# Optimization experiments

Measured on AMD Instinct MI355X. Metric: run time of the kernel, lower is better.

The kernel has to match this reference:

```python
import jax, jax.numpy as jnp
import numpy as np

B, O, H, I = 256, 128, 1024, 2048  # batch, objects, hidden, input_size
Hh = H // 2  # 512; x_j feature dim
DF = I - Hh  # 1536; X_F feature dim


def _xavier(key, shape):
    fan_in, fan_out = shape[1], shape[0]
    lim = np.sqrt(6.0 / (fan_in + fan_out))
    return jax.random.uniform(key, shape, jnp.float32, -lim, lim)


def setup_inputs() -> dict:
    key = jax.random.key(0)
    ks = jax.random.split(key, 24)
    mask = jax.random.bernoulli(ks[0], 0.7, (B, O))
    mask = mask.at[:, 0].set(True)  # ensure at least one valid object per row
    inp = {
        "x_j": jax.random.normal(ks[1], (B, O, Hh), jnp.float32),
        "x_mask": mask,
        "X_F": jax.random.normal(ks[2], (B, DF), jnp.float32),
        "h": jax.random.normal(ks[3], (B, 1, H), jnp.float32),
        "c": jax.random.normal(ks[4], (B, 1, H), jnp.float32),
    }
    names_W = ["W_i", "W_f", "W_c", "W_o"]
    names_U = ["U_i", "U_f", "U_c", "U_o"]
    names_V = ["V_i", "V_f", "V_c", "V_o"]
    k = 5
    for n in names_W:
        inp[n] = _xavier(ks[k], (H, I)); k += 1
    for n in names_U + names_V:
        inp[n] = _xavier(ks[k], (H, H)); k += 1
    for n in ["b_i", "b_f", "b_c", "b_o"]:
        inp[n] = jnp.zeros((H,), jnp.float32)
    inp["w"] = _xavier(ks[k], (1, Hh)); k += 1
    inp["W_e"] = _xavier(ks[k], (Hh, H)); k += 1
    inp["U_e"] = _xavier(ks[k], (Hh, Hh)); k += 1
    inp["b_e"] = jnp.zeros((Hh,), jnp.float32)
    return inp


def reference(x_j, x_mask, X_F, h, c,
              W_i, W_f, W_c, W_o,
              U_i, U_f, U_c, U_o,
              V_i, V_f, V_c, V_o,
              b_i, b_f, b_c, b_o,
              w, W_e, U_e, b_e):
    # Additive attention over objects.
    # h: (B,1,H) -> (B,1,Hh) broadcasts against x_j proj (B,O,Hh)
    e = jnp.tanh(h @ W_e.T + x_j @ U_e.T + b_e)      # (B,O,Hh)
    e = (e @ w.T)[..., 0]                              # (B,O)
    e = jnp.where(x_mask, e, -1e9)
    a = jax.nn.softmax(e, axis=1)                      # (B,O)
    phi_j = jnp.einsum('bo,bok->bk', a, x_j)[:, None, :]  # (B,1,Hh)
    x = jnp.concatenate([phi_j, X_F[:, None, :]], axis=2)  # (B,1,I)

    # Peephole LSTM gates (h, c: (B,1,H))
    i = jax.nn.sigmoid(x @ W_i.T + h @ U_i.T + c @ V_i.T + b_i)
    f = jax.nn.sigmoid(x @ W_f.T + h @ U_f.T + c @ V_f.T + b_f)
    new_c = f * c + i * jnp.tanh(x @ W_c.T + h @ U_c.T + b_c)
    o = jax.nn.sigmoid(x @ W_o.T + h @ U_o.T + c @ V_o.T + b_o)
    new_h = o * jnp.tanh(new_c)
    return new_h, new_c
```

## Files before the change

kernel.cpp:

```cpp
#include <hip/hip_runtime.h>
#include <hip/hip_bf16.h>

typedef unsigned char u8;
typedef unsigned short u16;
typedef unsigned int u32;
typedef __attribute__((ext_vector_type(8))) short bf8;
typedef __attribute__((ext_vector_type(4))) float f4;

#define B_ 256
#define O_ 128
#define Hh_ 512
#define H_ 1024
#define DF_ 1536
#define I_ 2048

#define HWE_OFF   0
#define XC_OFF    524288
#define PRE_OFF   2621440
#define FLAG_OFF  6815744

__device__ __forceinline__ float bflo(u32 u){ union{u32 i; float f;} v; v.i = u<<16; return v.f; }
__device__ __forceinline__ float bfhi(u32 u){ union{u32 i; float f;} v; v.i = u & 0xffff0000u; return v.f; }
__device__ __forceinline__ float bf1(u16 u){ union{u32 i; float f;} v; v.i = ((u32)u)<<16; return v.f; }
__device__ __forceinline__ u16 f2bf(float f){
    __hip_bfloat16 h = __float2bfloat16(f);
    union{ __hip_bfloat16 h; u16 u; } v; v.h = h; return v.u;
}
__device__ __forceinline__ u32 pack2(float a, float b){
    return ((u32)f2bf(a)) | (((u32)f2bf(b))<<16);
}
__device__ __forceinline__ uint4 load8(const void* p, size_t idx, int isf32){
    if(isf32){
        const float4* f = (const float4*)((const float*)p + idx);
        float4 x = f[0], y = f[1];
        uint4 r;
        r.x = pack2(x.x, x.y); r.y = pack2(x.z, x.w);
        r.z = pack2(y.x, y.y); r.w = pack2(y.z, y.w);
        return r;
    }
    return *(const uint4*)((const u16*)p + idx);
}
__device__ __forceinline__ float loads(const void* p, size_t idx, int isf32){
    return isf32 ? ((const float*)p)[idx] : bf1(((const u16*)p)[idx]);
}
__device__ __forceinline__ float fast_tanh(float x){
    return 1.0f - 2.0f/(__expf(2.0f*x)+1.0f);
}
__device__ __forceinline__ float sigmoidf_(float x){
    return 1.0f/(1.0f+__expf(-x));
}

__global__ void k_detect(const u8* __restrict__ m, const u16* __restrict__ xj,
                         int* __restrict__ flags){
    __shared__ int n1, n2, n3, mb, xo;
    int t = threadIdx.x;
    if(t==0){ n1=0; n2=0; n3=0; mb=0; xo=0; }
    __syncthreads();
    int a1=0, a2=0, a3=0, amax=0;
    for(int i=t; i<8192; i+=256){
        int v = m[i]; int c = i&3;
        if(c==1) a1|=v;
        if(c==2) a2|=v;
        if(c==3) a3|=v;
        amax = amax > v ? amax : v;
    }
    if(a1) atomicOr(&n1,1);
    if(a2) atomicOr(&n2,1);
    if(a3) atomicOr(&n3,1);
    atomicMax(&mb, amax);
    int e = 0;
    for(int i=t; i<2048; i+=256){
        u32 u = xj[2*i];
        int ex = (u>>7)&0xFF;
        if(ex >= 156) e = 1;
    }
    if(e) atomicOr(&xo,1);
    __syncthreads();
    if(t==0){
        int w;
        if(!n1 && !n2 && !n3)      w = 4;
        else if(!n1 && n2 && n3)   w = 4;
        else if(mb > 1)            w = 2;
        else                       w = 1;
        flags[0] = w;
        flags[1] = xo;
    }
}

__global__ __launch_bounds__(256) void k_hwe(const void* __restrict__ h,
                                             const void* __restrict__ We,
                                             const int* __restrict__ flags,
                                             float* __restrict__ hwe){
    int n0 = blockIdx.x*64;
    int kc = blockIdx.y*256;
    int m0 = blockIdx.z*128;
    int t = threadIdx.x;
    int isf32 = flags[1];
    __shared__ __align__(16) u16 As[128*40];
    __shared__ __align__(16) u16 Bs[64*40];
    int w = t>>6, lane = t&63;
    int q = lane>>4, l16 = lane&15;
    int koff = q*8;
    f4 acc[2][4];
    for(int mi=0;mi<2;mi++) for(int ni=0;ni<4;ni++){
        f4 z = {0.f,0.f,0.f,0.f}; acc[mi][ni] = z;
    }
    for(int ks=0; ks<256; ks+=32){
        __syncthreads();
        for(int i=0;i<2;i++){
            int row = i*64 + (t>>2), cv = t&3;
            uint4 va = load8(h, (size_t)(m0+row)*H_ + kc + ks + cv*8, isf32);
            *(uint4*)&As[row*40 + cv*8] = va;
        }
        {
            int row = t>>2, cv = t&3;
            uint4 vb = load8(We, (size_t)(n0+row)*H_ + kc + ks + cv*8, isf32);
            *(uint4*)&Bs[row*40 + cv*8] = vb;
        }
        __syncthreads();
        bf8 af[2], bfr[4];
        for(int mi=0;mi<2;mi++) af[mi]  = *(const bf8*)&As[(w*32+mi*16+l16)*40 + koff];
        for(int ni=0;ni<4;ni++) bfr[ni] = *(const bf8*)&Bs[(ni*16+l16)*40 + koff];
        for(int mi=0;mi<2;mi++)
            for(int ni=0;ni<4;ni++)
                acc[mi][ni] = __builtin_amdgcn_mfma_f32_16x16x32_bf16(af[mi], bfr[ni], acc[mi][ni], 0,0,0);
    }
    for(int mi=0;mi<2;mi++){
        for(int r=0;r<4;r++){
            int brow = m0 + w*32 + mi*16 + q*4 + r;
            for(int ni=0;ni<4;ni++){
                int ncol = n0 + ni*16 + l16;
                atomicAdd(&hwe[(size_t)brow*Hh_ + ncol], acc[mi][ni][r]);
            }
        }
    }
}

__global__ __launch_bounds__(256) void k_pack(const void* __restrict__ XF,
                                              const void* __restrict__ h,
                                              const void* __restrict__ c,
                                              const int* __restrict__ flags,
                                              u16* __restrict__ Xc){
    int b = blockIdx.y;
    int r = blockIdx.x*256 + threadIdx.x;
    int isf32 = flags[1];
    float v;
    if(r < DF_)            v = loads(XF, (size_t)b*DF_ + r, isf32);
    else if(r < DF_ + H_)  v = loads(h,  (size_t)b*H_ + (r - DF_), isf32);
    else                   v = loads(c,  (size_t)b*H_ + (r - DF_ - H_), isf32);
    Xc[(size_t)b*4096 + 512 + r] = f2bf(v);
}

__global__ __launch_bounds__(256) void k_attn(const void* __restrict__ xj,
                                              const void* __restrict__ wvec,
                                              const void* __restrict__ Ue,
                                              const void* __restrict__ be,
                                              const float* __restrict__ hwe,
                                              const int* __restrict__ flags,
                                              float* __restrict__ Epart){
    int b = blockIdx.x, nc = blockIdx.y, t = threadIdx.x;
    int isf32 = flags[1];
    __shared__ __align__(16) u16 As[128*40];
    __shared__ __align__(16) u16 Bs[128*40];
    __shared__ float hwes[128];
    __shared__ float wvs[128];
    __shared__ float es[O_];

    if(t < 128){
        int col = nc*128 + t;
        hwes[t] = hwe[(size_t)b*Hh_ + col] + loads(be, col, isf32);
        wvs[t]  = loads(wvec, col, isf32);
    }
    if(t < O_) es[t] = 0.f;

    const size_t xboff = (size_t)b*O_*Hh_;

    int w = t>>6, lane = t&63;
    int wm = w>>1, wn = w&1;
    int q = lane>>4, l16 = lane&15;
    int koff = q*8;

    f4 acc[4][4];
    for(int mi=0;mi<4;mi++) for(int ni=0;ni<4;ni++){
        f4 z = {0.f,0.f,0.f,0.f}; acc[mi][ni] = z;
    }
    for(int ks=0; ks<Hh_; ks+=32){
        __syncthreads();
        for(int i=0;i<2;i++){
            int qq = t + i*256;
            int row = qq>>2, cv = qq&3;
            uint4 va = load8(xj, xboff + (size_t)row*Hh_ + ks + cv*8, isf32);
            *(uint4*)&As[row*40 + cv*8] = va;
            uint4 vb = load8(Ue, (size_t)(nc*128 + row)*Hh_ + ks + cv*8, isf32);
            *(uint4*)&Bs[row*40 + cv*8] = vb;
        }
        __syncthreads();
        bf8 af[4], bfr[4];
        for(int mi=0;mi<4;mi++) af[mi]  = *(const bf8*)&As[(wm*64+mi*16+l16)*40 + koff];
        for(int ni=0;ni<4;ni++) bfr[ni] = *(const bf8*)&Bs[(wn*64+ni*16+l16)*40 + koff];
        for(int mi=0;mi<4;mi++)
            for(int ni=0;ni<4;ni++)
                acc[mi][ni] = __builtin_amdgcn_mfma_f32_16x16x32_bf16(af[mi], bfr[ni], acc[mi][ni], 0,0,0);
    }
    for(int mi=0;mi<4;mi++){
        for(int r=0;r<4;r++){
            int o = wm*64 + mi*16 + q*4 + r;
            float part = 0.f;
            for(int ni=0;ni<4;ni++){
                int col = wn*64 + ni*16 + l16;
                part += wvs[col] * fast_tanh(hwes[col] + acc[mi][ni][r]);
            }
            part += __shfl_xor(part, 1);
            part += __shfl_xor(part, 2);
            part += __shfl_xor(part, 4);
            part += __shfl_xor(part, 8);
            if(l16 == 0) atomicAdd(&es[o], part);
        }
    }
    __syncthreads();
    if(t < O_) Epart[(size_t)nc*32768 + (size_t)b*O_ + t] = es[t];
}

__global__ __launch_bounds__(512) void k_soft(const float* __restrict__ Epart,
                                              const void* __restrict__ maskp,
                                              const void* __restrict__ xj,
                                              const int* __restrict__ flags,
                                              u16* __restrict__ Xc){
    int b = blockIdx.x, t = threadIdx.x;
    int isf32 = flags[1];
    int mw = flags[0];
    __shared__ float es[O_];
    __shared__ float as_[O_];
    __shared__ float red[2];
    if(t < O_){
        float e = Epart[(size_t)b*O_ + t]
                + Epart[32768 + (size_t)b*O_ + t]
                + Epart[2*32768 + (size_t)b*O_ + t]
                + Epart[3*32768 + (size_t)b*O_ + t];
        size_t mi_ = (size_t)b*O_ + t;
        bool valid;
        if(mw == 1)      valid = ((const u8*)maskp)[mi_]  != 0;
        else if(mw == 2) valid = ((const u16*)maskp)[mi_] != 0;
        else             valid = ((const u32*)maskp)[mi_] != 0;
        es[t] = valid ? e : -1e30f;
    }
    __syncthreads();
    if(t < 64){
        float v = fmaxf(es[t], es[t+64]);
        for(int m=32;m>0;m>>=1) v = fmaxf(v, __shfl_xor(v, m));
        if(t==0) red[0] = v;
    }
    __syncthreads();
    if(t < O_) as_[t] = __expf(es[t] - red[0]);
    __syncthreads();
    if(t < 64){
        float v = as_[t] + as_[t+64];
        for(int m=32;m>0;m>>=1) v += __shfl_xor(v, m);
        if(t==0) red[1] = v;
    }
    __syncthreads();
    float inv = 1.0f / red[1];
    float acc = 0.f;
    size_t base = (size_t)b*O_*Hh_ + t;
    #pragma unroll 4
    for(int o=0;o<O_;o++){
        acc += as_[o] * loads(xj, base + (size_t)o*Hh_, isf32);
    }
    Xc[(size_t)b*4096 + t] = f2bf(acc * inv);
}

__global__ __launch_bounds__(512) void k_gates(const u16* __restrict__ Xc,
    const void* __restrict__ Wi, const void* __restrict__ Wf, const void* __restrict__ Wc, const void* __restrict__ Wo,
    const void* __restrict__ Ui, const void* __restrict__ Uf, const void* __restrict__ Uc, const void* __restrict__ Uo,
    const void* __restrict__ Vi, const void* __restrict__ Vf, const void* __restrict__ Vo,
    const int* __restrict__ flags,
    float* __restrict__ pre){
    int nt = blockIdx.x;
    int kc = blockIdx.y;
    int g  = nt>>4;
    if(g == 2 && kc == 3) return;
    int isf32 = flags[1];
    const void* Wm = (g==0)?Wi:(g==1)?Wf:(g==2)?Wc:Wo;
    const void* Um = (g==0)?Ui:(g==1)?Uf:(g==2)?Uc:Uo;
    const void* Vm = (g==0)?Vi:(g==1)?Vf:(g==3)?Vo:Vi;
    int n0 = (nt&15)*64;
    int k0 = kc*1024;
    int t = threadIdx.x;
    __shared__ __align__(16) u16 As[256*40];
    __shared__ __align__(16) u16 Bs[64*40];
    int w = t>>6, lane = t&63;
    int q = lane>>4, l16 = lane&15;
    int koff = q*8;
    f4 acc[2][4];
    for(int mi=0;mi<2;mi++) for(int ni=0;ni<4;ni++){
        f4 z = {0.f,0.f,0.f,0.f}; acc[mi][ni] = z;
    }
    for(int ks=0; ks<1024; ks+=32){
        __syncthreads();
        for(int i=0;i<2;i++){
            int row = i*128 + (t>>2), cv = t&3;
            uint4 va = *(const uint4*)(Xc + (size_t)row*4096 + k0 + ks + cv*8);
            *(uint4*)&As[row*40 + cv*8] = va;
        }
        if(t < 256){
            int row = t>>2, cv = t&3;
            int n = n0 + row;
            int k = k0 + ks + cv*8;
            uint4 vb;
            if(k < 2048)       vb = load8(Wm, (size_t)n*I_ + k, isf32);
            else if(k < 3072)  vb = load8(Um, (size_t)n*H_ + (k-2048), isf32);
            else               vb = load8(Vm, (size_t)n*H_ + (k-3072), isf32);
            *(uint4*)&Bs[row*40 + cv*8] = vb;
        }
        __syncthreads();
        bf8 af[2], bfr[4];
        for(int mi=0;mi<2;mi++) af[mi]  = *(const bf8*)&As[(w*32+mi*16+l16)*40 + koff];
        for(int ni=0;ni<4;ni++) bfr[ni] = *(const bf8*)&Bs[(ni*16+l16)*40 + koff];
        for(int mi=0;mi<2;mi++)
            for(int ni=0;ni<4;ni++)
                acc[mi][ni] = __builtin_amdgcn_mfma_f32_16x16x32_bf16(af[mi], bfr[ni], acc[mi][ni], 0,0,0);
    }
    float* pg = pre + (size_t)g*(B_*H_);
    for(int mi=0;mi<2;mi++){
        for(int r=0;r<4;r++){
            int brow = w*32 + mi*16 + q*4 + r;
            for(int ni=0;ni<4;ni++){
                int ncol = n0 + ni*16 + l16;
                atomicAdd(&pg[(size_t)brow*H_ + ncol], acc[mi][ni][r]);
            }
        }
    }
}

__global__ __launch_bounds__(256) void k_combine(const float* __restrict__ pre,
    const void* __restrict__ c,
    const void* __restrict__ bi, const void* __restrict__ bfv,
    const void* __restrict__ bc, const void* __restrict__ bo,
    const int* __restrict__ flags,
    float* __restrict__ out){
    int b = blockIdx.x, t = threadIdx.x;
    int isf32 = flags[1];
    const size_t G = (size_t)B_*H_;
    for(int i=0;i<4;i++){
        int n = i*256 + t;
        size_t idx = (size_t)b*H_ + n;
        float pi = pre[idx]       + loads(bi,  n, isf32);
        float pf = pre[G   + idx] + loads(bfv, n, isf32);
        float pc = pre[2*G + idx] + loads(bc,  n, isf32);
        float po = pre[3*G + idx] + loads(bo,  n, isf32);
        float ig = sigmoidf_(pi);
        float fg = sigmoidf_(pf);
        float og = sigmoidf_(po);
        float cold = loads(c, idx, isf32);
        float ncv = fg*cold + ig*fast_tanh(pc);
        float nh  = og*fast_tanh(ncv);
        out[idx]     = nh;
        out[G + idx] = ncv;
    }
}

extern "C" void kernel_launch(void* const* d_in, const int* in_sizes, int n_in,
                              void* d_out, int out_size, void* d_ws, size_t ws_size,
                              hipStream_t stream){
    const void* xj   = d_in[0];
    const void* mask = d_in[1];
    const void* XF   = d_in[2];
    const void* h    = d_in[3];
    const void* c    = d_in[4];
    const void* Wi   = d_in[5];
    const void* Wf   = d_in[6];
    const void* Wc   = d_in[7];
    const void* Wo   = d_in[8];
    const void* Ui   = d_in[9];
    const void* Uf   = d_in[10];
    const void* Uc   = d_in[11];
    const void* Uo   = d_in[12];
    const void* Vi   = d_in[13];
    const void* Vf   = d_in[14];
    const void* Vo   = d_in[16];
    const void* bi   = d_in[17];
    const void* bfv  = d_in[18];
    const void* bc   = d_in[19];
    const void* bo   = d_in[20];
    const void* wv   = d_in[21];
    const void* We   = d_in[22];
    const void* Ue   = d_in[23];
    const void* be   = d_in[24];

    char* ws = (char*)d_ws;
    float* hwe  = (float*)(ws + HWE_OFF);
    u16*   Xc   = (u16*)(ws + XC_OFF);
    float* pre  = (float*)(ws + PRE_OFF);
    int*   flags= (int*)(ws + FLAG_OFF);
    float* out  = (float*)d_out;

    k_detect<<<1, 256, 0, stream>>>((const u8*)mask, (const u16*)xj, flags);
    hipMemsetAsync(hwe, 0, (size_t)B_*Hh_*sizeof(float), stream);
    k_hwe<<<dim3(8,4,2), 256, 0, stream>>>(h, We, flags, hwe);
    k_pack<<<dim3(14, B_), 256, 0, stream>>>(XF, h, c, flags, Xc);
    k_attn<<<dim3(B_, 4), 256, 0, stream>>>(xj, wv, Ue, be, hwe, flags, pre);
    k_soft<<<B_, 512, 0, stream>>>(pre, mask, xj, flags, Xc);
    hipMemsetAsync(pre, 0, (size_t)4*B_*H_*sizeof(float), stream);
    k_gates<<<dim3(64, 4), 512, 0, stream>>>(Xc, Wi,Wf,Wc,Wo, Ui,Uf,Uc,Uo, Vi,Vf,Vo, flags, pre);
    k_combine<<<B_, 256, 0, stream>>>(pre, c, bi, bfv, bc, bo, flags, out);
}
```

Baseline: 346.3 us.

## Pre-convert x_j/U_e to bf16, register-prefetch tiles, and split more work

Adds a conversion kernel that writes bf16 copies of x_j and U_e into the workspace when it is large enough, so the attention and softmax kernels read half the bytes. The attention and gate GEMMs now fetch the next K tile into registers while the current one is being computed. The attention grid is split into 8 column chunks of 64 with direct partial writes. The hwe and gates kernels get finer K splits for more blocks. The extra conversion pass costs a full read and write of x_j, and the finer splits add more atomics and partial sums.

```diff
diff --git a/kernel.cpp b/kernel.cpp
--- a/kernel.cpp
+++ b/kernel.cpp
@@ -18,6 +18,9 @@
 #define XC_OFF    524288
 #define PRE_OFF   2621440
 #define FLAG_OFF  6815744
+#define XJ16_OFF  7340032
+#define UE16_OFF  40894464
+#define WS_BIG    41418752
 
 __device__ __forceinline__ float bflo(u32 u){ union{u32 i; float f;} v; v.i = u<<16; return v.f; }
 __device__ __forceinline__ float bfhi(u32 u){ union{u32 i; float f;} v; v.i = u & 0xffff0000u; return v.f; }
@@ -29,16 +32,29 @@
 __device__ __forceinline__ u32 pack2(float a, float b){
     return ((u32)f2bf(a)) | (((u32)f2bf(b))<<16);
 }
+struct P8 { uint4 lo, hi; };
+__device__ __forceinline__ P8 fetch8(const void* p, size_t idx, int isf32){
+    P8 r;
+    if(isf32){
+        const uint4* f = (const uint4*)((const float*)p + idx);
+        r.lo = f[0]; r.hi = f[1];
+    } else {
+        r.lo = *(const uint4*)((const u16*)p + idx);
+    }
+    return r;
+}
+__device__ __forceinline__ uint4 cvt8(P8 r, int isf32){
+    if(isf32){
+        float4 x = *(float4*)&r.lo, y = *(float4*)&r.hi;
+        uint4 o;
+        o.x = pack2(x.x,x.y); o.y = pack2(x.z,x.w);
+        o.z = pack2(y.x,y.y); o.w = pack2(y.z,y.w);
+        return o;
+    }
+    return r.lo;
+}
 __device__ __forceinline__ uint4 load8(const void* p, size_t idx, int isf32){
-    if(isf32){
-        const float4* f = (const float4*)((const float*)p + idx);
-        float4 x = f[0], y = f[1];
-        uint4 r;
-        r.x = pack2(x.x, x.y); r.y = pack2(x.z, x.w);
-        r.z = pack2(y.x, y.y); r.w = pack2(y.z, y.w);
-        return r;
-    }
-    return *(const uint4*)((const u16*)p + idx);
+    return cvt8(fetch8(p, idx, isf32), isf32);
 }
 __device__ __forceinline__ float loads(const void* p, size_t idx, int isf32){
     return isf32 ? ((const float*)p)[idx] : bf1(((const u16*)p)[idx]);
@@ -87,12 +103,28 @@
     }
 }
 
+__global__ __launch_bounds__(256) void k_conv(const void* __restrict__ xj,
+                                              const void* __restrict__ Ue,
+                                              const int* __restrict__ flags,
+                                              u16* __restrict__ xj16,
+                                              u16* __restrict__ ue16){
+    int isf32 = flags[1];
+    size_t g = (size_t)blockIdx.x*256 + threadIdx.x;
+    if(g < 2097152){
+        size_t idx = g*8;
+        *(uint4*)&xj16[idx] = load8(xj, idx, isf32);
+    } else {
+        size_t idx = (g - 2097152)*8;
+        *(uint4*)&ue16[idx] = load8(Ue, idx, isf32);
+    }
+}
+
 __global__ __launch_bounds__(256) void k_hwe(const void* __restrict__ h,
                                              const void* __restrict__ We,
                                              const int* __restrict__ flags,
                                              float* __restrict__ hwe){
     int n0 = blockIdx.x*64;
-    int kc = blockIdx.y*256;
+    int kc = blockIdx.y*128;
     int m0 = blockIdx.z*128;
     int t = threadIdx.x;
     int isf32 = flags[1];
@@ -105,7 +137,7 @@
     for(int mi=0;mi<2;mi++) for(int ni=0;ni<4;ni++){
         f4 z = {0.f,0.f,0.f,0.f}; acc[mi][ni] = z;
     }
-    for(int ks=0; ks<256; ks+=32){
+    for(int ks=0; ks<128; ks+=32){
         __syncthreads();
         for(int i=0;i<2;i++){
             int row = i*64 + (t>>2), cv = t&3;
@@ -151,92 +183,96 @@
     Xc[(size_t)b*4096 + 512 + r] = f2bf(v);
 }
 
-__global__ __launch_bounds__(256) void k_attn(const void* __restrict__ xj,
+__global__ __launch_bounds__(256) void k_attn(const void* __restrict__ xjA,
                                               const void* __restrict__ wvec,
-                                              const void* __restrict__ Ue,
+                                              const void* __restrict__ UeA,
                                               const void* __restrict__ be,
                                               const float* __restrict__ hwe,
                                               const int* __restrict__ flags,
+                                              int srcbf,
                                               float* __restrict__ Epart){
     int b = blockIdx.x, nc = blockIdx.y, t = threadIdx.x;
-    int isf32 = flags[1];
+    int isf = flags[1];
+    int isA = srcbf ? 0 : isf;
     __shared__ __align__(16) u16 As[128*40];
-    __shared__ __align__(16) u16 Bs[128*40];
-    __shared__ float hwes[128];
-    __shared__ float wvs[128];
-    __shared__ float es[O_];
-
-    if(t < 128){
-        int col = nc*128 + t;
-        hwes[t] = hwe[(size_t)b*Hh_ + col] + loads(be, col, isf32);
-        wvs[t]  = loads(wvec, col, isf32);
-    }
-    if(t < O_) es[t] = 0.f;
+    __shared__ __align__(16) u16 Bs[64*40];
+    __shared__ float hwes[64];
+    __shared__ float wvs[64];
+
+    if(t < 64){
+        int col = nc*64 + t;
+        hwes[t] = hwe[(size_t)b*Hh_ + col] + loads(be, col, isf);
+        wvs[t]  = loads(wvec, col, isf);
+    }
 
     const size_t xboff = (size_t)b*O_*Hh_;
-
     int w = t>>6, lane = t&63;
-    int wm = w>>1, wn = w&1;
     int q = lane>>4, l16 = lane&15;
     int koff = q*8;
-
-    f4 acc[4][4];
-    for(int mi=0;mi<4;mi++) for(int ni=0;ni<4;ni++){
+    int rA = t>>2, cA = t&3;
+
+    f4 acc[2][4];
+    for(int mi=0;mi<2;mi++) for(int ni=0;ni<4;ni++){
         f4 z = {0.f,0.f,0.f,0.f}; acc[mi][ni] = z;
     }
+
+    P8 pa0, pa1, pb;
+    pa0 = fetch8(xjA, xboff + (size_t)rA*Hh_      + cA*8, isA);
+    pa1 = fetch8(xjA, xboff + (size_t)(rA+64)*Hh_ + cA*8, isA);
+    pb  = fetch8(UeA, (size_t)(nc*64 + rA)*Hh_    + cA*8, isA);
+
     for(int ks=0; ks<Hh_; ks+=32){
         __syncthreads();
-        for(int i=0;i<2;i++){
-            int qq = t + i*256;
-            int row = qq>>2, cv = qq&3;
-            uint4 va = load8(xj, xboff + (size_t)row*Hh_ + ks + cv*8, isf32);
-            *(uint4*)&As[row*40 + cv*8] = va;
-            uint4 vb = load8(Ue, (size_t)(nc*128 + row)*Hh_ + ks + cv*8, isf32);
-            *(uint4*)&Bs[row*40 + cv*8] = vb;
-        }
-        __syncthreads();
-        bf8 af[4], bfr[4];
-        for(int mi=0;mi<4;mi++) af[mi]  = *(const bf8*)&As[(wm*64+mi*16+l16)*40 + koff];
-        for(int ni=0;ni<4;ni++) bfr[ni] = *(const bf8*)&Bs[(wn*64+ni*16+l16)*40 + koff];
-        for(int mi=0;mi<4;mi++)
+        *(uint4*)&As[rA*40 + cA*8]      = cvt8(pa0, isA);
+        *(uint4*)&As[(rA+64)*40 + cA*8] = cvt8(pa1, isA);
+        *(uint4*)&Bs[rA*40 + cA*8]      = cvt8(pb, isA);
+        __syncthreads();
+        if(ks + 32 < Hh_){
+            int kn = ks + 32;
+            pa0 = fetch8(xjA, xboff + (size_t)rA*Hh_      + kn + cA*8, isA);
+            pa1 = fetch8(xjA, xboff + (size_t)(rA+64)*Hh_ + kn + cA*8, isA);
+            pb  = fetch8(UeA, (size_t)(nc*64 + rA)*Hh_    + kn + cA*8, isA);
+        }
+        bf8 af[2], bfr[4];
+        for(int mi=0;mi<2;mi++) af[mi]  = *(const bf8*)&As[(w*32+mi*16+l16)*40 + koff];
+        for(int ni=0;ni<4;ni++) bfr[ni] = *(const bf8*)&Bs[(ni*16+l16)*40 + koff];
+        for(int mi=0;mi<2;mi++)
             for(int ni=0;ni<4;ni++)
                 acc[mi][ni] = __builtin_amdgcn_mfma_f32_16x16x32_bf16(af[mi], bfr[ni], acc[mi][ni], 0,0,0);
     }
-    for(int mi=0;mi<4;mi++){
+    for(int mi=0;mi<2;mi++){
         for(int r=0;r<4;r++){
-            int o = wm*64 + mi*16 + q*4 + r;
+            int o = w*32 + mi*16 + q*4 + r;
             float part = 0.f;
             for(int ni=0;ni<4;ni++){
-                int col = wn*64 + ni*16 + l16;
+                int col = ni*16 + l16;
                 part += wvs[col] * fast_tanh(hwes[col] + acc[mi][ni][r]);
             }
             part += __shfl_xor(part, 1);
             part += __shfl_xor(part, 2);
             part += __shfl_xor(part, 4);
             part += __shfl_xor(part, 8);
-            if(l16 == 0) atomicAdd(&es[o], part);
-        }
-    }
-    __syncthreads();
-    if(t < O_) Epart[(size_t)nc*32768 + (size_t)b*O_ + t] = es[t];
+            if(l16 == 0) Epart[(size_t)nc*32768 + (size_t)b*O_ + o] = part;
+        }
+    }
 }
 
 __global__ __launch_bounds__(512) void k_soft(const float* __restrict__ Epart,
                                               const void* __restrict__ maskp,
-                                              const void* __restrict__ xj,
+                                              const void* __restrict__ xjA,
                                               const int* __restrict__ flags,
+                                              int srcbf,
                                               u16* __restrict__ Xc){
     int b = blockIdx.x, t = threadIdx.x;
-    int isf32 = flags[1];
+    int isf = flags[1];
+    int isA = srcbf ? 0 : isf;
     int mw = flags[0];
     __shared__ float es[O_];
     __shared__ float as_[O_];
     __shared__ float red[2];
     if(t < O_){
-        float e = Epart[(size_t)b*O_ + t]
-                + Epart[32768 + (size_t)b*O_ + t]
-                + Epart[2*32768 + (size_t)b*O_ + t]
-                + Epart[3*32768 + (size_t)b*O_ + t];
+        float e = 0.f;
+        for(int p=0;p<8;p++) e += Epart[(size_t)p*32768 + (size_t)b*O_ + t];
         size_t mi_ = (size_t)b*O_ + t;
         bool valid;
         if(mw == 1)      valid = ((const u8*)maskp)[mi_]  != 0;
@@ -262,9 +298,9 @@
     float inv = 1.0f / red[1];
     float acc = 0.f;
     size_t base = (size_t)b*O_*Hh_ + t;
-    #pragma unroll 4
+    #pragma unroll 8
     for(int o=0;o<O_;o++){
-        acc += as_[o] * loads(xj, base + (size_t)o*Hh_, isf32);
+        acc += as_[o] * loads(xjA, base + (size_t)o*Hh_, isA);
     }
     Xc[(size_t)b*4096 + t] = f2bf(acc * inv);
 }
@@ -278,41 +314,51 @@
     int nt = blockIdx.x;
     int kc = blockIdx.y;
     int g  = nt>>4;
-    if(g == 2 && kc == 3) return;
+    int k0 = kc*512;
+    if(g == 2 && k0 >= 3072) return;
     int isf32 = flags[1];
     const void* Wm = (g==0)?Wi:(g==1)?Wf:(g==2)?Wc:Wo;
     const void* Um = (g==0)?Ui:(g==1)?Uf:(g==2)?Uc:Uo;
     const void* Vm = (g==0)?Vi:(g==1)?Vf:(g==3)?Vo:Vi;
     int n0 = (nt&15)*64;
-    int k0 = kc*1024;
     int t = threadIdx.x;
     __shared__ __align__(16) u16 As[256*40];
     __shared__ __align__(16) u16 Bs[64*40];
     int w = t>>6, lane = t&63;
     int q = lane>>4, l16 = lane&15;
     int koff = q*8;
+    int rA = t>>2, cA = t&3;
+    bool hasB = (t < 256);
+
     f4 acc[2][4];
     for(int mi=0;mi<2;mi++) for(int ni=0;ni<4;ni++){
         f4 z = {0.f,0.f,0.f,0.f}; acc[mi][ni] = z;
     }
-    for(int ks=0; ks<1024; ks+=32){
-        __syncthreads();
-        for(int i=0;i<2;i++){
-            int row = i*128 + (t>>2), cv = t&3;
-            uint4 va = *(const uint4*)(Xc + (size_t)row*4096 + k0 + ks + cv*8);
-            *(uint4*)&As[row*40 + cv*8] = va;
-        }
-        if(t < 256){
-            int row = t>>2, cv = t&3;
-            int n = n0 + row;
-            int k = k0 + ks + cv*8;
-            uint4 vb;
-            if(k < 2048)       vb = load8(Wm, (size_t)n*I_ + k, isf32);
-            else if(k < 3072)  vb = load8(Um, (size_t)n*H_ + (k-2048), isf32);
-            else               vb = load8(Vm, (size_t)n*H_ + (k-3072), isf32);
-            *(uint4*)&Bs[row*40 + cv*8] = vb;
-        }
-        __syncthreads();
+
+    auto fetchB = [&](int k)->P8{
+        int n = n0 + rA;
+        if(k < 2048)       return fetch8(Wm, (size_t)n*I_ + k, isf32);
+        else if(k < 3072)  return fetch8(Um, (size_t)n*H_ + (k-2048), isf32);
+        else               return fetch8(Vm, (size_t)n*H_ + (k-3072), isf32);
+    };
+
+    uint4 qa0, qa1; P8 qb;
+    qa0 = *(const uint4*)(Xc + (size_t)rA*4096       + k0 + cA*8);
+    qa1 = *(const uint4*)(Xc + (size_t)(rA+128)*4096 + k0 + cA*8);
+    if(hasB) qb = fetchB(k0 + cA*8);
+
+    for(int ks=0; ks<512; ks+=32){
+        __syncthreads();
+        *(uint4*)&As[rA*40 + cA*8]       = qa0;
+        *(uint4*)&As[(rA+128)*40 + cA*8] = qa1;
+        if(hasB) *(uint4*)&Bs[rA*40 + cA*8] = cvt8(qb, isf32);
+        __syncthreads();
+        if(ks + 32 < 512){
+            int kn = k0 + ks + 32;
+            qa0 = *(const uint4*)(Xc + (size_t)rA*4096       + kn + cA*8);
+            qa1 = *(const uint4*)(Xc + (size_t)(rA+128)*4096 + kn + cA*8);
+            if(hasB) qb = fetchB(kn + cA*8);
+        }
         bf8 af[2], bfr[4];
         for(int mi=0;mi<2;mi++) af[mi]  = *(const bf8*)&As[(w*32+mi*16+l16)*40 + koff];
         for(int ni=0;ni<4;ni++) bfr[ni] = *(const bf8*)&Bs[(ni*16+l16)*40 + koff];
@@ -394,13 +440,20 @@
     int*   flags= (int*)(ws + FLAG_OFF);
     float* out  = (float*)d_out;
 
+    int big = (ws_size >= (size_t)WS_BIG);
+    u16* xj16 = (u16*)(ws + XJ16_OFF);
+    u16* ue16 = (u16*)(ws + UE16_OFF);
+    const void* xjA = big ? (const void*)xj16 : xj;
+    const void* UeA = big ? (const void*)ue16 : Ue;
+
     k_detect<<<1, 256, 0, stream>>>((const u8*)mask, (const u16*)xj, flags);
     hipMemsetAsync(hwe, 0, (size_t)B_*Hh_*sizeof(float), stream);
-    k_hwe<<<dim3(8,4,2), 256, 0, stream>>>(h, We, flags, hwe);
+    if(big) k_conv<<<8320, 256, 0, stream>>>(xj, Ue, flags, xj16, ue16);
+    k_hwe<<<dim3(8,8,2), 256, 0, stream>>>(h, We, flags, hwe);
     k_pack<<<dim3(14, B_), 256, 0, stream>>>(XF, h, c, flags, Xc);
-    k_attn<<<dim3(B_, 4), 256, 0, stream>>>(xj, wv, Ue, be, hwe, flags, pre);
-    k_soft<<<B_, 512, 0, stream>>>(pre, mask, xj, flags, Xc);
+    k_attn<<<dim3(B_, 8), 256, 0, stream>>>(xjA, wv, UeA, be, hwe, flags, big, pre);
+    k_soft<<<B_, 512, 0, stream>>>(pre, mask, xjA, flags, big, Xc);
     hipMemsetAsync(pre, 0, (size_t)4*B_*H_*sizeof(float), stream);
-    k_gates<<<dim3(64, 4), 512, 0, stream>>>(Xc, Wi,Wf,Wc,Wo, Ui,Uf,Uc,Uo, Vi,Vf,Vo, flags, pre);
+    k_gates<<<dim3(64, 8), 512, 0, stream>>>(Xc, Wi,Wf,Wc,Wo, Ui,Uf,Uc,Uo, Vi,Vf,Vo, flags, pre);
     k_combine<<<B_, 256, 0, stream>>>(pre, c, bi, bfv, bc, bo, flags, out);
 }
```

New measurement: 338.6 us. 1.02x faster.
